# Kernel tuning notes

Measured on AMD Instinct MI355X. Metric: run time of the kernel, lower is better.

The kernel has to match this reference:

```python
import jax, jax.numpy as jnp
import numpy as np

NU = 160000   # users
NM = 60000    # movies
D = 64        # embedding dim
E = 5000000   # rating edges
L = 200000    # label edges to score
NUM_LAYERS = 3


def setup_inputs() -> dict:
    key = jax.random.key(0)
    k1, k2, k3, k4, k5, k6 = jax.random.split(key, 6)
    return {
        "emb_user": jax.random.normal(k1, (NU, D), jnp.float32),
        "emb_movie": jax.random.normal(k2, (NM, D), jnp.float32),
        "node_id_user": jnp.arange(NU),
        "node_id_movie": jnp.arange(NM),
        "edge_from": jax.random.randint(k3, (E,), 0, NM),   # movie side of each edge
        "edge_to": jax.random.randint(k4, (E,), 0, NU),     # user side of each edge
        "label_movie": jax.random.randint(k5, (L,), 0, NM),
        "label_user": jax.random.randint(k6, (L,), 0, NU),
    }


def reference(emb_user, emb_movie, node_id_user, node_id_movie,
              edge_from, edge_to, label_movie, label_user):
    # Embedding lookup (node_id is an arange over all nodes in the batch)
    x_u = emb_user[node_id_user]    # [NU, D]
    x_m = emb_movie[node_id_movie]  # [NM, D]

    # Symmetric degree normalization: deg(from)^-1/2 * deg(to)^-1/2 per edge
    ones = jnp.ones(edge_from.shape[0], dtype=x_m.dtype)
    deg_m = jax.ops.segment_sum(ones, edge_from, num_segments=NM)
    deg_u = jax.ops.segment_sum(ones, edge_to, num_segments=NU)
    inv_m = jnp.where(deg_m > 0, deg_m ** -0.5, 0.0)
    inv_u = jnp.where(deg_u > 0, deg_u ** -0.5, 0.0)
    norm = inv_m[edge_from] * inv_u[edge_to]  # [E]

    # NOTE: the original torch code never writes the propagated embeddings back
    # into x_dict, so every layer propagates the layer-0 embeddings. Replicated
    # faithfully here.
    embs_u = [x_u]
    embs_m = [x_m]
    for _ in range(NUM_LAYERS):
        # movie -> user aggregation (x2y): gather movie feats, scale, scatter-add to users
        u_agg = jax.ops.segment_sum(norm[:, None] * x_m[edge_from], edge_to, num_segments=NU)
        m_agg = jax.ops.segment_sum(norm[:, None] * x_u[edge_to], edge_from, num_segments=NM)
        embs_u.append(u_agg)
        embs_m.append(m_agg)

    # Layer combination with weights 1/(l+1)
    w = 1.0 / (jnp.arange(NUM_LAYERS + 1, dtype=x_u.dtype) + 1.0)
    res_u = jnp.einsum('l,lnd->nd', w, jnp.stack(embs_u))  # [NU, D]
    res_m = jnp.einsum('l,lnd->nd', w, jnp.stack(embs_m))  # [NM, D]

    # Classifier: dot product over label edges
    scores = jnp.sum(res_u[label_user] * res_m[label_movie], axis=-1)  # [L]
    return (scores, res_u, res_m)
```

## Files before the change

kernel.cpp:

```cpp
#include <hip/hip_runtime.h>
#include <hip/hip_bf16.h>

#define NU 160000
#define NM 60000
#define DD 64
#define NE 5000000
#define NL 200000

#define COEF (13.0f / 12.0f)

#define GU 20
#define NPH_U 4
#define UDIV 15000
#define NGRP_U (NU / GU)
#define NVK_U (NGRP_U * NPH_U * GU)
#define NBK_U ((NVK_U + 1023) >> 10)

#define GM 8
#define NPH_M 10
#define MDIV 16000
#define NGRP_M (NM / GM)
#define NVK_M (NGRP_M * NPH_M * GM)
#define NBK_M ((NVK_M + 1023) >> 10)

#define VB_U 16
#define VB_M 18
#define BS 1024


#define CEC 16

__device__ __forceinline__ int vk_u_of(int u, int m) {
    return ((u / GU) * NPH_U + m / UDIV) * GU + (u % GU);
}
__device__ __forceinline__ int vk_m_of(int m, int u) {
    return (((m >> 3) * NPH_M) + u / MDIV) * GM + (m & 7);
}

__global__ void bucket_count_kernel(const int* __restrict__ ef, const int* __restrict__ et,
                                    int* __restrict__ gbh_u, int* __restrict__ gbh_m) {
    __shared__ int bhu[NBK_U], bhm[NBK_M];
    int tid = threadIdx.x;
    for (int i = tid; i < NBK_U; i += 256) bhu[i] = 0;
    for (int i = tid; i < NBK_M; i += 256) bhm[i] = 0;
    __syncthreads();
    int base = (blockIdx.x * 256 + tid) * CEC;
    if (base < NE) {
        const int4* f4 = (const int4*)(ef + base);
        const int4* t4 = (const int4*)(et + base);
        #pragma unroll
        for (int q = 0; q < CEC / 4; q++) {
            int4 ff = f4[q]; int4 tt = t4[q];
            atomicAdd(&bhm[vk_m_of(ff.x, tt.x) >> 10], 1); atomicAdd(&bhu[vk_u_of(tt.x, ff.x) >> 10], 1);
            atomicAdd(&bhm[vk_m_of(ff.y, tt.y) >> 10], 1); atomicAdd(&bhu[vk_u_of(tt.y, ff.y) >> 10], 1);
            atomicAdd(&bhm[vk_m_of(ff.z, tt.z) >> 10], 1); atomicAdd(&bhu[vk_u_of(tt.z, ff.z) >> 10], 1);
            atomicAdd(&bhm[vk_m_of(ff.w, tt.w) >> 10], 1); atomicAdd(&bhu[vk_u_of(tt.w, ff.w) >> 10], 1);
        }
    }
    __syncthreads();
    for (int i = tid; i < NBK_U; i += 256) if (bhu[i]) atomicAdd(&gbh_u[i], bhu[i]);
    for (int i = tid; i < NBK_M; i += 256) if (bhm[i]) atomicAdd(&gbh_m[i], bhm[i]);
}


__global__ void scan_small_kernel(const int* __restrict__ in, int* __restrict__ out,
                                  int* __restrict__ cur, int n) {
    __shared__ int buf[256];
    int tid = threadIdx.x;
    int idx = tid * 4;
    int v0 = (idx + 0 < n) ? in[idx + 0] : 0;
    int v1 = (idx + 1 < n) ? in[idx + 1] : 0;
    int v2 = (idx + 2 < n) ? in[idx + 2] : 0;
    int v3 = (idx + 3 < n) ? in[idx + 3] : 0;
    int s = v0 + v1 + v2 + v3;
    buf[tid] = s;
    __syncthreads();
    for (int off = 1; off < 256; off <<= 1) {
        int t = (tid >= off) ? buf[tid - off] : 0;
        __syncthreads();
        buf[tid] += t;
        __syncthreads();
    }
    int p = buf[tid] - s;
    if (idx + 0 < n) { out[idx + 0] = p; if (cur) cur[idx + 0] = p; p += v0; }
    if (idx + 1 < n) { out[idx + 1] = p; if (cur) cur[idx + 1] = p; p += v1; }
    if (idx + 2 < n) { out[idx + 2] = p; if (cur) cur[idx + 2] = p; p += v2; }
    if (idx + 3 < n) { out[idx + 3] = p; if (cur) cur[idx + 3] = p; p += v3; }
    if (tid == 255) out[n] = buf[255];
}


#define PEC 16

__global__ void partition_kernel(const int* __restrict__ key, const int* __restrict__ val,
                                 int* __restrict__ bcur, int* __restrict__ stage,
                                 int nb, int valbits, int mode) {
    __shared__ int lh[1024];
    __shared__ int lbase[1024];
    int tid = threadIdx.x;
    for (int i = tid; i < nb; i += 256) lh[i] = 0;
    __syncthreads();
    int base = (blockIdx.x * 256 + tid) * PEC;
    int lk_[PEC], v_[PEC], br_[PEC];
    bool act = base < NE;
    if (act) {
        int k_[PEC];
        const int4* k4 = (const int4*)(key + base);
        const int4* v4 = (const int4*)(val + base);
        #pragma unroll
        for (int q = 0; q < PEC / 4; q++) {
            int4 kk = k4[q]; int4 vv = v4[q];
            k_[q * 4 + 0] = kk.x; k_[q * 4 + 1] = kk.y; k_[q * 4 + 2] = kk.z; k_[q * 4 + 3] = kk.w;
            v_[q * 4 + 0] = vv.x; v_[q * 4 + 1] = vv.y; v_[q * 4 + 2] = vv.z; v_[q * 4 + 3] = vv.w;
        }
        #pragma unroll
        for (int q = 0; q < PEC; q++) {
            int vk = (mode == 0) ? vk_u_of(k_[q], v_[q]) : vk_m_of(k_[q], v_[q]);
            lk_[q] = vk & 1023;
            int b = vk >> 10;
            int r = atomicAdd(&lh[b], 1);
            br_[q] = (b << 13) | r;
        }
    }
    __syncthreads();
    for (int i = tid; i < nb; i += 256) lbase[i] = lh[i] ? atomicAdd(&bcur[i], lh[i]) : 0;
    __syncthreads();
    if (act) {
        #pragma unroll
        for (int q = 0; q < PEC; q++) {
            int b = br_[q] >> 13;
            int r = br_[q] & 8191;
            stage[lbase[b] + r] = (lk_[q] << valbits) | v_[q];
        }
    }
}


__global__ void build_kernel(const int* __restrict__ stage, const int* __restrict__ bo,
                             int* __restrict__ rp, int* __restrict__ pay,
                             int n, int valbits) {
    __shared__ int cnt[BS];
    __shared__ int tmp[BS];
    int b = blockIdx.x;
    int tid = threadIdx.x;
    int base = b << 10;
    int nn = min(BS, n - base);
    int vmask = (1 << valbits) - 1;
    int s0 = bo[b];
    int s1 = bo[b + 1];

    for (int i = tid; i < BS; i += 256) cnt[i] = 0;
    __syncthreads();
    for (int e = s0 + tid; e < s1; e += 256)
        atomicAdd(&cnt[stage[e] >> valbits], 1);
    __syncthreads();
    int ov[4];
    #pragma unroll
    for (int q = 0; q < 4; q++) ov[q] = cnt[tid + q * 256];
    for (int off = 1; off < BS; off <<= 1) {
        int t[4];
        #pragma unroll
        for (int q = 0; q < 4; q++) {
            int i = tid + q * 256;
            t[q] = (i >= off) ? cnt[i - off] : 0;
        }
        __syncthreads();
        #pragma unroll
        for (int q = 0; q < 4; q++) cnt[tid + q * 256] += t[q];
        __syncthreads();
    }
    #pragma unroll
    for (int q = 0; q < 4; q++) {
        int i = tid + q * 256;
        int excl = cnt[i] - ov[q];
        tmp[i] = s0 + excl;
        if (i < nn) rp[base + i] = s0 + excl;
    }
    if (b == 0 && tid == 0) rp[n] = NE;
    __syncthreads();
    for (int e = s0 + tid; e < s1; e += 256) {
        int p = stage[e];
        int pos = atomicAdd(&tmp[p >> valbits], 1);
        pay[pos] = p & vmask;
    }
}


__global__ void inv_u_kernel(const int* __restrict__ rp, float* __restrict__ inv) {
    int u = blockIdx.x * blockDim.x + threadIdx.x;
    if (u < NU) {
        int g = u / GU, i = u % GU;
        int d = 0;
        #pragma unroll
        for (int h = 0; h < NPH_U; h++) {
            int vk = (g * NPH_U + h) * GU + i;
            d += rp[vk + 1] - rp[vk];
        }
        inv[u] = (d > 0) ? rsqrtf((float)d) : 0.0f;
    }
}

__global__ void inv_m_kernel(const int* __restrict__ rp, float* __restrict__ inv) {
    int m = blockIdx.x * blockDim.x + threadIdx.x;
    if (m < NM) {
        int g = m >> 3, i = m & 7;
        int d = 0;
        #pragma unroll
        for (int h = 0; h < NPH_M; h++) {
            int vk = (g * NPH_M + h) * GM + i;
            d += rp[vk + 1] - rp[vk];
        }
        inv[m] = (d > 0) ? rsqrtf((float)d) : 0.0f;
    }
}


__global__ void prescale_kernel(const float* __restrict__ x, const float* __restrict__ inv,
                                __hip_bfloat16* __restrict__ y, int total) {
    int i = blockIdx.x * blockDim.x + threadIdx.x;
    if (i < total) {
        int node = i >> 6;
        y[i] = __float2bfloat16(inv[node] * x[i]);
    }
}


template <int G, int NPH>
__global__ __launch_bounds__(256, 8) void gather_kernel_t(
        const int* __restrict__ rp, const int* __restrict__ pay,
        const float* __restrict__ inv_dst,
        const __hip_bfloat16* __restrict__ y_src,
        const float* __restrict__ x_dst,
        float* __restrict__ res) {
    __shared__ float accL[4 * G * DD];
    int wslot = threadIdx.x >> 6;
    int lane = threadIdx.x & 63;
    int W = blockIdx.x * 4 + wslot;
    float* myacc = &accL[wslot * G * DD + lane];
    for (int i = 0; i < G; i++) myacc[i * DD] = 0.0f;

    int rr = 0;
    if (lane <= G) rr = rp[(W * NPH) * G + lane];
    for (int h = 0; h < NPH; h++) {
        int rrn = 0;
        if (h + 1 < NPH && lane <= G) rrn = rp[(W * NPH + h + 1) * G + lane];
        int sph = __shfl(rr, 0, 64);
        int eph = __shfl(rr, G, 64);
        int wbase = sph;
        int pv  = (wbase + lane      < eph) ? pay[wbase + lane]      : 0;
        int pv2 = (wbase + 64 + lane < eph) ? pay[wbase + 64 + lane] : 0;
        for (int i = 0; i < G; i++) {
            int s = __shfl(rr, i, 64);
            int e = __shfl(rr, i + 1, 64);
            float racc = 0.0f;
            while (s < e) {
                if (s >= wbase + 64) {
                    wbase += 64;
                    pv = pv2;
                    pv2 = (wbase + 64 + lane < eph) ? pay[wbase + 64 + lane] : 0;
                }
                int tend = min(e, wbase + 64);
                int j = s;
                for (; j + 8 <= tend; j += 8) {
                    int r = j - wbase;
                    int p0 = __shfl(pv, r + 0, 64);
                    int p1 = __shfl(pv, r + 1, 64);
                    int p2 = __shfl(pv, r + 2, 64);
                    int p3 = __shfl(pv, r + 3, 64);
                    int p4 = __shfl(pv, r + 4, 64);
                    int p5 = __shfl(pv, r + 5, 64);
                    int p6 = __shfl(pv, r + 6, 64);
                    int p7 = __shfl(pv, r + 7, 64);
                    float a0 = __bfloat162float(y_src[p0 * DD + lane]);
                    float a1 = __bfloat162float(y_src[p1 * DD + lane]);
                    float a2 = __bfloat162float(y_src[p2 * DD + lane]);
                    float a3 = __bfloat162float(y_src[p3 * DD + lane]);
                    float a4 = __bfloat162float(y_src[p4 * DD + lane]);
                    float a5 = __bfloat162float(y_src[p5 * DD + lane]);
                    float a6 = __bfloat162float(y_src[p6 * DD + lane]);
                    float a7 = __bfloat162float(y_src[p7 * DD + lane]);
                    racc += ((a0 + a1) + (a2 + a3)) + ((a4 + a5) + (a6 + a7));
                }
                if (j + 4 <= tend) {
                    int r = j - wbase;
                    int p0 = __shfl(pv, r + 0, 64);
                    int p1 = __shfl(pv, r + 1, 64);
                    int p2 = __shfl(pv, r + 2, 64);
                    int p3 = __shfl(pv, r + 3, 64);
                    float a0 = __bfloat162float(y_src[p0 * DD + lane]);
                    float a1 = __bfloat162float(y_src[p1 * DD + lane]);
                    float a2 = __bfloat162float(y_src[p2 * DD + lane]);
                    float a3 = __bfloat162float(y_src[p3 * DD + lane]);
                    racc += (a0 + a1) + (a2 + a3);
                    j += 4;
                }
                for (; j < tend; j++)
                    racc += __bfloat162float(y_src[__shfl(pv, j - wbase, 64) * DD + lane]);
                s = tend;
            }
            myacc[i * DD] += racc;
        }
        rr = rrn;
    }

    int g0 = W * G;
    for (int i = 0; i < G; i++) {
        int n = g0 + i;
        int o = n * DD + lane;
        res[o] = x_dst[o] + COEF * inv_dst[n] * myacc[i * DD];
    }
}


__global__ void score_kernel(const int* __restrict__ lm, const int* __restrict__ lu,
                             const float* __restrict__ ru, const float* __restrict__ rm,
                             float* __restrict__ scores) {
    int tid = blockIdx.x * blockDim.x + threadIdx.x;
    int l = tid >> 6;
    int d = threadIdx.x & 63;
    if (l < NL) {
        int u = lu[l];
        int m = lm[l];
        float v = ru[u * DD + d] * rm[m * DD + d];
        #pragma unroll
        for (int off = 32; off >= 1; off >>= 1)
            v += __shfl_down(v, off, 64);
        if (d == 0) scores[l] = v;
    }
}


__global__ void degree_kernel_f(const int* __restrict__ ef, const int* __restrict__ et,
                                float* __restrict__ deg_m, float* __restrict__ deg_u) {
    int i = blockIdx.x * blockDim.x + threadIdx.x;
    if (i < NE) {
        atomicAdd(&deg_m[ef[i]], 1.0f);
        atomicAdd(&deg_u[et[i]], 1.0f);
    }
}

__global__ void inv_kernel_f(float* __restrict__ deg, int n) {
    int i = blockIdx.x * blockDim.x + threadIdx.x;
    if (i < n) {
        float d = deg[i];
        deg[i] = (d > 0.0f) ? (1.0f / sqrtf(d)) : 0.0f;
    }
}

__global__ void agg_kernel_f(const int* __restrict__ ef, const int* __restrict__ et,
                             const float* __restrict__ inv_m, const float* __restrict__ inv_u,
                             const float* __restrict__ x_u, const float* __restrict__ x_m,
                             float* __restrict__ res_u, float* __restrict__ res_m) {
    int tid = blockIdx.x * blockDim.x + threadIdx.x;
    int e = tid >> 6;
    int d = tid & 63;
    if (e < NE) {
        int f = ef[e];
        int t = et[e];
        float norm = inv_m[f] * inv_u[t] * COEF;
        atomicAdd(&res_u[t * DD + d], norm * x_m[f * DD + d]);
        atomicAdd(&res_m[f * DD + d], norm * x_u[t * DD + d]);
    }
}

__global__ void add_base_kernel_f(const float* __restrict__ xu, const float* __restrict__ xm,
                                  float* __restrict__ ru, float* __restrict__ rm) {
    int i = blockIdx.x * blockDim.x + threadIdx.x;
    const int nu = NU * DD;
    const int nm = NM * DD;
    if (i < nu) {
        ru[i] += xu[i];
    } else if (i < nu + nm) {
        int j = i - nu;
        rm[j] += xm[j];
    }
}


extern "C" void kernel_launch(void* const* d_in, const int* in_sizes, int n_in,
                              void* d_out, int out_size, void* d_ws, size_t ws_size,
                              hipStream_t stream) {
    const float* emb_user  = (const float*)d_in[0];
    const float* emb_movie = (const float*)d_in[1];
    const int* edge_from   = (const int*)d_in[4];
    const int* edge_to     = (const int*)d_in[5];
    const int* label_movie = (const int*)d_in[6];
    const int* label_user  = (const int*)d_in[7];

    float* out    = (float*)d_out;
    float* scores = out;
    float* res_u  = out + NL;
    float* res_m  = out + NL + (size_t)NU * DD;

    int*   gbh_u  = (int*)d_ws;
    int*   gbh_m  = gbh_u + NBK_U;
    int*   bo_u   = gbh_m + NBK_M;
    int*   bcur_u = bo_u + NBK_U + 1;
    int*   bo_m   = bcur_u + NBK_U;
    int*   bcur_m = bo_m + NBK_M + 1;
    float* inv_u  = (float*)(bcur_m + NBK_M);
    float* inv_m  = inv_u + NU;
    int*   rp_u   = (int*)(inv_m + NM);
    int*   rp_m   = rp_u + NVK_U + 1;
    int*   pay_u  = rp_m + NVK_M + 1;
    int*   pay_m  = pay_u + NE;
    int*   ureg   = pay_m + NE;
    int*   stage  = ureg;
    __hip_bfloat16* y_u = (__hip_bfloat16*)ureg;
    __hip_bfloat16* y_m = (__hip_bfloat16*)(ureg + (size_t)NU * DD / 2);

    size_t ysz    = (size_t)(NU + NM) * DD / 2;
    size_t uni    = (size_t)NE > ysz ? (size_t)NE : ysz;
    size_t needed = ((size_t)(ureg - (int*)d_ws) + uni) * sizeof(int);

    if (ws_size >= needed) {
        hipMemsetAsync(gbh_u, 0, (size_t)(NBK_U + NBK_M) * sizeof(int), stream);

        bucket_count_kernel<<<(NE / CEC + 255) / 256, 256, 0, stream>>>(
            edge_from, edge_to, gbh_u, gbh_m);
        scan_small_kernel<<<1, 256, 0, stream>>>(gbh_u, bo_u, bcur_u, NBK_U);
        scan_small_kernel<<<1, 256, 0, stream>>>(gbh_m, bo_m, bcur_m, NBK_M);

        partition_kernel<<<(NE / PEC + 255) / 256, 256, 0, stream>>>(
            edge_to, edge_from, bcur_u, stage, NBK_U, VB_U, 0);
        build_kernel<<<NBK_U, 256, 0, stream>>>(stage, bo_u, rp_u, pay_u, NVK_U, VB_U);

        partition_kernel<<<(NE / PEC + 255) / 256, 256, 0, stream>>>(
            edge_from, edge_to, bcur_m, stage, NBK_M, VB_M, 1);
        build_kernel<<<NBK_M, 256, 0, stream>>>(stage, bo_m, rp_m, pay_m, NVK_M, VB_M);

        inv_u_kernel<<<(NU + 255) / 256, 256, 0, stream>>>(rp_u, inv_u);
        inv_m_kernel<<<(NM + 255) / 256, 256, 0, stream>>>(rp_m, inv_m);

        prescale_kernel<<<((size_t)NU * DD + 255) / 256, 256, 0, stream>>>(
            emb_user, inv_u, y_u, NU * DD);
        prescale_kernel<<<((size_t)NM * DD + 255) / 256, 256, 0, stream>>>(
            emb_movie, inv_m, y_m, NM * DD);

        gather_kernel_t<GU, NPH_U><<<NGRP_U / 4, 256, 0, stream>>>(
            rp_u, pay_u, inv_u, y_m, emb_user, res_u);
        gather_kernel_t<GM, NPH_M><<<NGRP_M / 4, 256, 0, stream>>>(
            rp_m, pay_m, inv_m, y_u, emb_movie, res_m);
    } else {
        float* fdeg_u = (float*)d_ws;
        float* fdeg_m = fdeg_u + NU;
        hipMemsetAsync(res_u, 0, (size_t)(NU + NM) * DD * sizeof(float), stream);
        hipMemsetAsync(fdeg_u, 0, (size_t)(NU + NM) * sizeof(float), stream);
        degree_kernel_f<<<(NE + 255) / 256, 256, 0, stream>>>(edge_from, edge_to, fdeg_m, fdeg_u);
        inv_kernel_f<<<(NU + NM + 255) / 256, 256, 0, stream>>>(fdeg_u, NU + NM);
        agg_kernel_f<<<((size_t)NE * 64 + 255) / 256, 256, 0, stream>>>(
            edge_from, edge_to, fdeg_m, fdeg_u, emb_user, emb_movie, res_u, res_m);
        add_base_kernel_f<<<((NU + NM) * DD + 255) / 256, 256, 0, stream>>>(
            emb_user, emb_movie, res_u, res_m);
    }

    score_kernel<<<((size_t)NL * 64 + 255) / 256, 256, 0, stream>>>(
        label_movie, label_user, res_u, res_m, scores);
}
```

Measured before the change: 773.8 us.

## Gather bf16 rows with 8-byte vector loads across 4 edges per wave

Restructures the CSR gather so each wave splits into four 16-lane groups, each loading 4 bf16 values (8 bytes) per lane for a different edge, which quadruples bytes per load instruction and processes 8 edges per iteration with masked weights. Per-group partial sums are combined via LDS atomicAdd into the shared accumulator. The rolling two-chunk payload window is replaced by per-row chunk loads of the payload, which may re-read payload indices and adds masked work for short rows.

```diff
diff --git a/kernel.cpp b/kernel.cpp
--- a/kernel.cpp
+++ b/kernel.cpp
@@ -235,70 +235,53 @@
     __shared__ float accL[4 * G * DD];
     int wslot = threadIdx.x >> 6;
     int lane = threadIdx.x & 63;
+    int grp = lane >> 4;
+    int q   = lane & 15;
     int W = blockIdx.x * 4 + wslot;
-    float* myacc = &accL[wslot * G * DD + lane];
-    for (int i = 0; i < G; i++) myacc[i * DD] = 0.0f;
+    float* myacc = &accL[wslot * G * DD];
+    for (int i = lane; i < G * DD; i += 64) myacc[i] = 0.0f;
+
+    const char* ybq = (const char*)y_src + (q << 3);
 
     int rr = 0;
     if (lane <= G) rr = rp[(W * NPH) * G + lane];
     for (int h = 0; h < NPH; h++) {
         int rrn = 0;
         if (h + 1 < NPH && lane <= G) rrn = rp[(W * NPH + h + 1) * G + lane];
-        int sph = __shfl(rr, 0, 64);
-        int eph = __shfl(rr, G, 64);
-        int wbase = sph;
-        int pv  = (wbase + lane      < eph) ? pay[wbase + lane]      : 0;
-        int pv2 = (wbase + 64 + lane < eph) ? pay[wbase + 64 + lane] : 0;
         for (int i = 0; i < G; i++) {
             int s = __shfl(rr, i, 64);
             int e = __shfl(rr, i + 1, 64);
-            float racc = 0.0f;
-            while (s < e) {
-                if (s >= wbase + 64) {
-                    wbase += 64;
-                    pv = pv2;
-                    pv2 = (wbase + 64 + lane < eph) ? pay[wbase + 64 + lane] : 0;
+            if (s == e) continue;
+            float r0 = 0.f, r1 = 0.f, r2 = 0.f, r3 = 0.f;
+            for (int c = s; c < e; c += 64) {
+                int cnt = min(e - c, 64);
+                int pvec = (lane < cnt) ? pay[c + lane] : 0;
+                for (int t = 0; t < cnt; t += 8) {
+                    int pA = __shfl(pvec, t + grp, 64);
+                    int pB = __shfl(pvec, (t + 4 + grp) & 63, 64);
+                    float wA = (t + grp < cnt) ? 1.0f : 0.0f;
+                    float wB = (t + 4 + grp < cnt) ? 1.0f : 0.0f;
+                    uint2 dA = *(const uint2*)(ybq + ((size_t)(unsigned)pA << 7));
+                    uint2 dB = *(const uint2*)(ybq + ((size_t)(unsigned)pB << 7));
+                    float a0 = __uint_as_float(dA.x << 16);
+                    float a1 = __uint_as_float(dA.x & 0xffff0000u);
+                    float a2 = __uint_as_float(dA.y << 16);
+                    float a3 = __uint_as_float(dA.y & 0xffff0000u);
+                    float b0 = __uint_as_float(dB.x << 16);
+                    float b1 = __uint_as_float(dB.x & 0xffff0000u);
+                    float b2 = __uint_as_float(dB.y << 16);
+                    float b3 = __uint_as_float(dB.y & 0xffff0000u);
+                    r0 = fmaf(a0, wA, r0); r1 = fmaf(a1, wA, r1);
+                    r2 = fmaf(a2, wA, r2); r3 = fmaf(a3, wA, r3);
+                    r0 = fmaf(b0, wB, r0); r1 = fmaf(b1, wB, r1);
+                    r2 = fmaf(b2, wB, r2); r3 = fmaf(b3, wB, r3);
                 }
-                int tend = min(e, wbase + 64);
-                int j = s;
-                for (; j + 8 <= tend; j += 8) {
-                    int r = j - wbase;
-                    int p0 = __shfl(pv, r + 0, 64);
-                    int p1 = __shfl(pv, r + 1, 64);
-                    int p2 = __shfl(pv, r + 2, 64);
-                    int p3 = __shfl(pv, r + 3, 64);
-                    int p4 = __shfl(pv, r + 4, 64);
-                    int p5 = __shfl(pv, r + 5, 64);
-                    int p6 = __shfl(pv, r + 6, 64);
-                    int p7 = __shfl(pv, r + 7, 64);
-                    float a0 = __bfloat162float(y_src[p0 * DD + lane]);
-                    float a1 = __bfloat162float(y_src[p1 * DD + lane]);
-                    float a2 = __bfloat162float(y_src[p2 * DD + lane]);
-                    float a3 = __bfloat162float(y_src[p3 * DD + lane]);
-                    float a4 = __bfloat162float(y_src[p4 * DD + lane]);
-                    float a5 = __bfloat162float(y_src[p5 * DD + lane]);
-                    float a6 = __bfloat162float(y_src[p6 * DD + lane]);
-                    float a7 = __bfloat162float(y_src[p7 * DD + lane]);
-                    racc += ((a0 + a1) + (a2 + a3)) + ((a4 + a5) + (a6 + a7));
-                }
-                if (j + 4 <= tend) {
-                    int r = j - wbase;
-                    int p0 = __shfl(pv, r + 0, 64);
-                    int p1 = __shfl(pv, r + 1, 64);
-                    int p2 = __shfl(pv, r + 2, 64);
-                    int p3 = __shfl(pv, r + 3, 64);
-                    float a0 = __bfloat162float(y_src[p0 * DD + lane]);
-                    float a1 = __bfloat162float(y_src[p1 * DD + lane]);
-                    float a2 = __bfloat162float(y_src[p2 * DD + lane]);
-                    float a3 = __bfloat162float(y_src[p3 * DD + lane]);
-                    racc += (a0 + a1) + (a2 + a3);
-                    j += 4;
-                }
-                for (; j < tend; j++)
-                    racc += __bfloat162float(y_src[__shfl(pv, j - wbase, 64) * DD + lane]);
-                s = tend;
             }
-            myacc[i * DD] += racc;
+            float* ap = &myacc[i * DD + (q << 2)];
+            atomicAdd(ap + 0, r0);
+            atomicAdd(ap + 1, r1);
+            atomicAdd(ap + 2, r2);
+            atomicAdd(ap + 3, r3);
         }
         rr = rrn;
     }
@@ -307,7 +290,7 @@
     for (int i = 0; i < G; i++) {
         int n = g0 + i;
         int o = n * DD + lane;
-        res[o] = x_dst[o] + COEF * inv_dst[n] * myacc[i * DD];
+        res[o] = x_dst[o] + COEF * inv_dst[n] * myacc[i * DD + lane];
     }
 }
 
```

After: 2.232 ms. +188.5%, slower.
